# Performance work log

Measured on AMD Instinct MI355X. Metric: run time of the kernel, lower is better.

Reference implementation:

```python
import jax, jax.numpy as jnp
import numpy as np

K_H, K_W = 3, 3
STRIDE, PAD = 1, 1
GN_GROUPS = 32
EPS = 1e-5


def setup_inputs() -> dict:
    key = jax.random.key(0)
    k1, k2, k3 = jax.random.split(key, 3)
    B, C, H, W = 4, 256, 64, 64
    Cout = 256
    x = jax.random.normal(k1, (B, C, H, W), jnp.float32)
    offset = jax.random.normal(k2, (B, 2 * K_H * K_W, H, W), jnp.float32)
    weight = jax.random.normal(k3, (Cout, C, K_H, K_W), jnp.float32) * 0.02
    gamma = jnp.ones((Cout,), jnp.float32)
    beta = jnp.zeros((Cout,), jnp.float32)
    return {"x": x, "offset": offset, "weight": weight, "gamma": gamma, "beta": beta}


def _deform_conv(x, offset, weight):
    B, C, H, W = x.shape
    Cout = weight.shape[0]
    K = K_H * K_W
    Ho = (H + 2 * PAD - K_H) // STRIDE + 1
    Wo = (W + 2 * PAD - K_W) // STRIDE + 1
    ky, kx = jnp.meshgrid(jnp.arange(K_H), jnp.arange(K_W), indexing='ij')
    ky = ky.reshape(K).astype(x.dtype)
    kx = kx.reshape(K).astype(x.dtype)
    # base sampling positions per kernel tap
    py_base = (jnp.arange(Ho) * STRIDE - PAD).astype(x.dtype)[None, :] + ky[:, None]  # [K,Ho]
    px_base = (jnp.arange(Wo) * STRIDE - PAD).astype(x.dtype)[None, :] + kx[:, None]  # [K,Wo]
    off = offset.reshape(B, K, 2, Ho, Wo)  # mmcv layout: (dy, dx) pairs per tap
    py = py_base[None, :, :, None] + off[:, :, 0]  # [B,K,Ho,Wo]
    px = px_base[None, :, None, :] + off[:, :, 1]  # [B,K,Ho,Wo]
    y0 = jnp.floor(py)
    x0 = jnp.floor(px)
    ly = py - y0
    lx = px - x0
    xf = x.reshape(B, C, H * W)

    def gather(yi, xi):
        valid = (yi >= 0) & (yi <= H - 1) & (xi >= 0) & (xi <= W - 1)
        yc = jnp.clip(yi, 0, H - 1).astype(jnp.int32)
        xc = jnp.clip(xi, 0, W - 1).astype(jnp.int32)
        idx = yc * W + xc  # [B,K,Ho,Wo]
        vals = jax.vmap(lambda xb, ib: xb[:, ib])(xf, idx)  # [B,C,K,Ho,Wo]
        return vals * valid[:, None].astype(x.dtype)

    g00 = gather(y0, x0)
    g01 = gather(y0, x0 + 1)
    g10 = gather(y0 + 1, x0)
    g11 = gather(y0 + 1, x0 + 1)
    wy = ly[:, None]  # [B,1,K,Ho,Wo]
    wx = lx[:, None]
    val = ((1 - wy) * (1 - wx) * g00 + (1 - wy) * wx * g01
           + wy * (1 - wx) * g10 + wy * wx * g11)  # [B,C,K,Ho,Wo]
    return jnp.einsum('bckhw,ock->bohw', val, weight.reshape(Cout, C, K))


def reference(x, offset, weight, gamma, beta):
    y = _deform_conv(x, offset, weight)  # [B,Cout,Ho,Wo]
    B, C, H, W = y.shape
    yg = y.reshape(B, GN_GROUPS, C // GN_GROUPS, H, W)
    mean = jnp.mean(yg, axis=(2, 3, 4), keepdims=True)
    var = jnp.var(yg, axis=(2, 3, 4), keepdims=True)
    yn = ((yg - mean) * jax.lax.rsqrt(var + EPS)).reshape(B, C, H, W)
    out = yn * gamma[None, :, None, None] + beta[None, :, None, None]
    return jax.nn.relu(out)
```

## Files before the change

kernel.cpp:

```cpp
#include <hip/hip_runtime.h>

typedef unsigned short ushort_t;
typedef __bf16 bf16x8 __attribute__((ext_vector_type(8)));
typedef float f32x4 __attribute__((ext_vector_type(4)));
typedef void __attribute__((address_space(1))) gvoid_t;
typedef void __attribute__((address_space(3))) lvoid_t;

__device__ __forceinline__ float bflo(unsigned u) { return __builtin_bit_cast(float, u << 16); }
__device__ __forceinline__ float bfhi(unsigned u) { return __builtin_bit_cast(float, u & 0xffff0000u); }
__device__ __forceinline__ unsigned f2bf_bits(float f) {
  unsigned u = __builtin_bit_cast(unsigned, f);
  return (u + 0x7fffu + ((u >> 16) & 1u)) >> 16;
}
__device__ __forceinline__ ushort_t f2bf(float f) { return (ushort_t)f2bf_bits(f); }

__global__ __launch_bounds__(256) void k_prep_w(const float* __restrict__ w,
                                                ushort_t* __restrict__ wb) {
  const int idx = blockIdx.x * 256 + threadIdx.x;
  const float* src = w + (size_t)idx * 9;
  #pragma unroll
  for (int k = 0; k < 9; ++k)
    wb[(k << 16) + idx] = f2bf(src[k]);
}

__global__ __launch_bounds__(256) void k_prep_x(const float* __restrict__ x,
                                                ushort_t* __restrict__ xt) {
  __shared__ ushort_t tile[64][68];
  const int bid = blockIdx.x;
  const int b = bid >> 8;
  const int ct = (bid >> 6) & 3;
  const int pt = bid & 63;
  const int t = threadIdx.x;
  const float* xb = x + ((size_t)(b * 256 + ct * 64)) * 4096 + pt * 64;
  #pragma unroll
  for (int i = 0; i < 16; ++i) {
    const int idx = t + 256 * i;
    const int c_l = idx >> 6, p_l = idx & 63;
    tile[c_l][p_l] = f2bf(xb[(size_t)c_l * 4096 + p_l]);
  }
  __syncthreads();
  ushort_t* xo = xt + ((size_t)(b * 4096 + pt * 64)) * 256 + ct * 64;
  #pragma unroll
  for (int i = 0; i < 16; ++i) {
    const int idx = t + 256 * i;
    const int p_l = idx >> 6, c_l = idx & 63;
    xo[(size_t)p_l * 256 + c_l] = tile[c_l][p_l];
  }
}

__global__ __launch_bounds__(256) void k_gemm(const float* __restrict__ off,
                                              const ushort_t* __restrict__ xt,
                                              const ushort_t* __restrict__ wb,
                                              float* __restrict__ y) {
  __shared__ __attribute__((aligned(16))) ushort_t Abuf[64 * 64];
  __shared__ __attribute__((aligned(16))) ushort_t Bbuf[256 * 64];

  const int bid = blockIdx.x;
  const int b = bid >> 6;
  const int h = bid & 63;
  const int t = threadIdx.x;
  const int wave = t >> 6;
  const int lane = t & 63;
  const int wq = lane >> 4;
  const int wr = lane & 15;

  const int s_w = t >> 2;
  const int c4i = t & 3;

  const f32x4 zero = {0.f, 0.f, 0.f, 0.f};
  f32x4 acc[4][4];
  #pragma unroll
  for (int i = 0; i < 4; ++i)
    #pragma unroll
    for (int j = 0; j < 4; ++j) acc[i][j] = zero;

  const float* offb = off + (size_t)b * 18 * 4096 + h * 64 + s_w;
  const ushort_t* xtb = xt + (size_t)b * 4096 * 256;

  for (int k = 0; k < 9; ++k) {
    const float offy = offb[(2 * k) * 4096];
    const float offx = offb[(2 * k + 1) * 4096];
    const float py = (float)(h - 1 + k / 3) + offy;
    const float px = (float)(s_w - 1 + k % 3) + offx;
    const float fy = floorf(py), fx = floorf(px);
    const float ly = py - fy, lx = px - fx;
    const int iy0 = (int)fy, ix0 = (int)fx;
    const float vy0 = (iy0 >= 0 && iy0 < 64) ? 1.f : 0.f;
    const float vy1 = (iy0 >= -1 && iy0 < 63) ? 1.f : 0.f;
    const float vx0 = (ix0 >= 0 && ix0 < 64) ? 1.f : 0.f;
    const float vx1 = (ix0 >= -1 && ix0 < 63) ? 1.f : 0.f;
    const float w00 = (1.f - ly) * (1.f - lx) * vy0 * vx0;
    const float w01 = (1.f - ly) * lx * vy0 * vx1;
    const float w10 = ly * (1.f - lx) * vy1 * vx0;
    const float w11 = ly * lx * vy1 * vx1;
    const int cy0 = min(max(iy0, 0), 63), cy1 = min(max(iy0 + 1, 0), 63);
    const int cx0 = min(max(ix0, 0), 63), cx1 = min(max(ix0 + 1, 0), 63);
    const ushort_t* p00 = xtb + (cy0 * 64 + cx0) * 256;
    const ushort_t* p01 = xtb + (cy0 * 64 + cx1) * 256;
    const ushort_t* p10 = xtb + (cy1 * 64 + cx0) * 256;
    const ushort_t* p11 = xtb + (cy1 * 64 + cx1) * 256;

    for (int c0 = 0; c0 < 256; c0 += 64) {
      __syncthreads();
      #pragma unroll
      for (int hf = 0; hf < 2; ++hf) {
        const int cc = c0 + hf * 32 + c4i * 8;
        const uint4 q00 = *(const uint4*)(p00 + cc);
        const uint4 q01 = *(const uint4*)(p01 + cc);
        const uint4 q10 = *(const uint4*)(p10 + cc);
        const uint4 q11 = *(const uint4*)(p11 + cc);
        uint4 r;
        {
          float lo = w00 * bflo(q00.x) + w01 * bflo(q01.x) + w10 * bflo(q10.x) + w11 * bflo(q11.x);
          float hi = w00 * bfhi(q00.x) + w01 * bfhi(q01.x) + w10 * bfhi(q10.x) + w11 * bfhi(q11.x);
          r.x = f2bf_bits(lo) | (f2bf_bits(hi) << 16);
        }
        {
          float lo = w00 * bflo(q00.y) + w01 * bflo(q01.y) + w10 * bflo(q10.y) + w11 * bflo(q11.y);
          float hi = w00 * bfhi(q00.y) + w01 * bfhi(q01.y) + w10 * bfhi(q10.y) + w11 * bfhi(q11.y);
          r.y = f2bf_bits(lo) | (f2bf_bits(hi) << 16);
        }
        {
          float lo = w00 * bflo(q00.z) + w01 * bflo(q01.z) + w10 * bflo(q10.z) + w11 * bflo(q11.z);
          float hi = w00 * bfhi(q00.z) + w01 * bfhi(q01.z) + w10 * bfhi(q10.z) + w11 * bfhi(q11.z);
          r.z = f2bf_bits(lo) | (f2bf_bits(hi) << 16);
        }
        {
          float lo = w00 * bflo(q00.w) + w01 * bflo(q01.w) + w10 * bflo(q10.w) + w11 * bflo(q11.w);
          float hi = w00 * bfhi(q00.w) + w01 * bfhi(q01.w) + w10 * bfhi(q10.w) + w11 * bfhi(q11.w);
          r.w = f2bf_bits(lo) | (f2bf_bits(hi) << 16);
        }
        const int slot = (hf * 4 + c4i) ^ (s_w & 7);
        *(uint4*)&Abuf[s_w * 64 + slot * 8] = r;
      }
      #pragma unroll
      for (int i = 0; i < 8; ++i) {
        const int row = i * 32 + (t >> 3);
        const int slot = t & 7;
        const int cl = ((slot ^ (row & 7)) << 3);
        const ushort_t* g = wb + (((k << 8) + row) << 8) + c0 + cl;
        __builtin_amdgcn_global_load_lds((gvoid_t*)g,
                                         (lvoid_t*)((char*)Bbuf + i * 4096 + t * 16),
                                         16, 0, 0);
      }
      __syncthreads();
      #pragma unroll
      for (int ks = 0; ks < 2; ++ks) {
        bf16x8 af[4], bfr[4];
        #pragma unroll
        for (int tm = 0; tm < 4; ++tm) {
          const int row = tm * 16 + wr;
          const int slot = (ks * 4 + wq) ^ (row & 7);
          af[tm] = *(const bf16x8*)&Abuf[row * 64 + slot * 8];
        }
        #pragma unroll
        for (int tn = 0; tn < 4; ++tn) {
          const int row = wave * 64 + tn * 16 + wr;
          const int slot = (ks * 4 + wq) ^ (row & 7);
          bfr[tn] = *(const bf16x8*)&Bbuf[row * 64 + slot * 8];
        }
        #pragma unroll
        for (int tm = 0; tm < 4; ++tm)
          #pragma unroll
          for (int tn = 0; tn < 4; ++tn)
            acc[tm][tn] =
                __builtin_amdgcn_mfma_f32_16x16x32_bf16(af[tm], bfr[tn], acc[tm][tn], 0, 0, 0);
      }
    }
  }
  float* yb = y + ((size_t)(b * 4096 + h * 64)) * 256;
  #pragma unroll
  for (int tm = 0; tm < 4; ++tm) {
    #pragma unroll
    for (int tn = 0; tn < 4; ++tn) {
      const int o = wave * 64 + tn * 16 + wr;
      #pragma unroll
      for (int r2 = 0; r2 < 4; ++r2) {
        const int ww = tm * 16 + wq * 4 + r2;
        yb[ww * 256 + o] = acc[tm][tn][r2];
      }
    }
  }
}

__global__ __launch_bounds__(256) void k_stats(const float* __restrict__ y,
                                               float* __restrict__ stats) {
  const int bid = blockIdx.x;
  const int b = bid >> 3, ch = bid & 7;
  const int t = threadIdx.x;
  float sum = 0.f, ss = 0.f;
  const float* p = y + ((size_t)(b * 4096 + ch * 512)) * 256 + t;
  for (int s = 0; s < 512; ++s) {
    const float v = p[(size_t)s * 256];
    sum += v;
    ss += v * v;
  }
  #pragma unroll
  for (int d = 1; d < 8; d <<= 1) {
    sum += __shfl_xor(sum, d, 64);
    ss += __shfl_xor(ss, d, 64);
  }
  if ((t & 7) == 0) {
    const int g = t >> 3;
    atomicAdd(&stats[(b * 32 + g) * 2], sum);
    atomicAdd(&stats[(b * 32 + g) * 2 + 1], ss);
  }
}

__global__ __launch_bounds__(256) void k_apply(const float* __restrict__ y,
                                               const float* __restrict__ stats,
                                               const float* __restrict__ gamma,
                                               const float* __restrict__ beta,
                                               float* __restrict__ out) {
  __shared__ float tile[64][65];
  __shared__ float sm[8], sr[8], sg[64], sb[64];
  const int bid = blockIdx.x;
  const int b = bid >> 8;
  const int st = (bid >> 2) & 63;
  const int ot = bid & 3;
  const int t = threadIdx.x;
  if (t < 8) {
    const int g = ot * 8 + t;
    const float s1 = stats[(b * 32 + g) * 2];
    const float s2 = stats[(b * 32 + g) * 2 + 1];
    const float mean = s1 * (1.f / 32768.f);
    const float var = s2 * (1.f / 32768.f) - mean * mean;
    sm[t] = mean;
    sr[t] = rsqrtf(var + 1e-5f);
  }
  if (t < 64) {
    sg[t] = gamma[ot * 64 + t];
    sb[t] = beta[ot * 64 + t];
  }
  const float* yb = y + ((size_t)(b * 4096 + st * 64)) * 256 + ot * 64;
  #pragma unroll
  for (int i = 0; i < 16; ++i) {
    const int idx = t + 256 * i;
    const int s_l = idx >> 6, o_l = idx & 63;
    tile[s_l][o_l] = yb[(size_t)s_l * 256 + o_l];
  }
  __syncthreads();
  float* ob = out + ((size_t)(b * 256 + ot * 64)) * 4096 + st * 64;
  #pragma unroll
  for (int i = 0; i < 16; ++i) {
    const int idx = t + 256 * i;
    const int o_l = idx >> 6, s_l = idx & 63;
    const int g = o_l >> 3;
    float v = (tile[s_l][o_l] - sm[g]) * sr[g] * sg[o_l] + sb[o_l];
    v = v > 0.f ? v : 0.f;
    ob[(size_t)o_l * 4096 + s_l] = v;
  }
}

extern "C" void kernel_launch(void* const* d_in, const int* in_sizes, int n_in,
                              void* d_out, int out_size, void* d_ws, size_t ws_size,
                              hipStream_t stream) {
  const float* x = (const float*)d_in[0];
  const float* off = (const float*)d_in[1];
  const float* w = (const float*)d_in[2];
  const float* gamma = (const float*)d_in[3];
  const float* beta = (const float*)d_in[4];
  float* out = (float*)d_out;

  char* ws = (char*)d_ws;
  float* y = (float*)(ws);
  ushort_t* xt = (ushort_t*)(ws + 16777216);
  ushort_t* wb = (ushort_t*)(ws + 25165824);
  float* stats = (float*)(ws + 26345472);

  hipMemsetAsync(stats, 0, 1024, stream);
  k_prep_w<<<256, 256, 0, stream>>>(w, wb);
  k_prep_x<<<1024, 256, 0, stream>>>(x, xt);
  k_gemm<<<256, 256, 0, stream>>>(off, xt, wb, y);
  k_stats<<<32, 256, 0, stream>>>(y, stats);
  k_apply<<<1024, 256, 0, stream>>>(y, stats, gamma, beta, out);
}
```

Baseline: 100.6 us.

## Fuse group-norm statistics into GEMM epilogue and halve GEMM row tile

Removes the separate k_stats kernel: the GEMM epilogue now reduces per-group sum and sum of squares from its accumulators with wave shuffles and atomically adds them to the stats buffer. The GEMM tile also shrinks from 64 to 32 output pixels per block, doubling the grid to 512 blocks, which fills more of the CUs. In exchange each block reloads the full weight tile for half the output pixels, and atomic traffic on the stats buffer rises.

Result: slower. 110.1 us (+9.5%).

```diff
diff --git a/kernel.cpp b/kernel.cpp
--- a/kernel.cpp
+++ b/kernel.cpp
@@ -51,37 +51,40 @@
 __global__ __launch_bounds__(256) void k_gemm(const float* __restrict__ off,
                                               const ushort_t* __restrict__ xt,
                                               const ushort_t* __restrict__ wb,
-                                              float* __restrict__ y) {
-  __shared__ __attribute__((aligned(16))) ushort_t Abuf[64 * 64];
+                                              float* __restrict__ y,
+                                              float* __restrict__ stats) {
+  __shared__ __attribute__((aligned(16))) ushort_t Abuf[32 * 64];
   __shared__ __attribute__((aligned(16))) ushort_t Bbuf[256 * 64];
 
   const int bid = blockIdx.x;
-  const int b = bid >> 6;
-  const int h = bid & 63;
+  const int b = bid >> 7;
+  const int h = (bid >> 1) & 63;
+  const int wh = bid & 1;
   const int t = threadIdx.x;
   const int wave = t >> 6;
   const int lane = t & 63;
   const int wq = lane >> 4;
   const int wr = lane & 15;
 
-  const int s_w = t >> 2;
-  const int c4i = t & 3;
+  const int s_w = t >> 3;
+  const int c8 = t & 7;
 
   const f32x4 zero = {0.f, 0.f, 0.f, 0.f};
-  f32x4 acc[4][4];
-  #pragma unroll
-  for (int i = 0; i < 4; ++i)
+  f32x4 acc[2][4];
+  #pragma unroll
+  for (int i = 0; i < 2; ++i)
     #pragma unroll
     for (int j = 0; j < 4; ++j) acc[i][j] = zero;
 
-  const float* offb = off + (size_t)b * 18 * 4096 + h * 64 + s_w;
+  const int gw = wh * 32 + s_w;
+  const float* offb = off + (size_t)b * 18 * 4096 + h * 64 + gw;
   const ushort_t* xtb = xt + (size_t)b * 4096 * 256;
 
   for (int k = 0; k < 9; ++k) {
     const float offy = offb[(2 * k) * 4096];
     const float offx = offb[(2 * k + 1) * 4096];
     const float py = (float)(h - 1 + k / 3) + offy;
-    const float px = (float)(s_w - 1 + k % 3) + offx;
+    const float px = (float)(gw - 1 + k % 3) + offx;
     const float fy = floorf(py), fx = floorf(px);
     const float ly = py - fy, lx = px - fx;
     const int iy0 = (int)fy, ix0 = (int)fx;
@@ -102,9 +105,8 @@
 
     for (int c0 = 0; c0 < 256; c0 += 64) {
       __syncthreads();
-      #pragma unroll
-      for (int hf = 0; hf < 2; ++hf) {
-        const int cc = c0 + hf * 32 + c4i * 8;
+      {
+        const int cc = c0 + c8 * 8;
         const uint4 q00 = *(const uint4*)(p00 + cc);
         const uint4 q01 = *(const uint4*)(p01 + cc);
         const uint4 q10 = *(const uint4*)(p10 + cc);
@@ -130,7 +132,7 @@
           float hi = w00 * bfhi(q00.w) + w01 * bfhi(q01.w) + w10 * bfhi(q10.w) + w11 * bfhi(q11.w);
           r.w = f2bf_bits(lo) | (f2bf_bits(hi) << 16);
         }
-        const int slot = (hf * 4 + c4i) ^ (s_w & 7);
+        const int slot = c8 ^ (s_w & 7);
         *(uint4*)&Abuf[s_w * 64 + slot * 8] = r;
       }
       #pragma unroll
@@ -146,9 +148,9 @@
       __syncthreads();
       #pragma unroll
       for (int ks = 0; ks < 2; ++ks) {
-        bf16x8 af[4], bfr[4];
+        bf16x8 af[2], bfr[4];
         #pragma unroll
-        for (int tm = 0; tm < 4; ++tm) {
+        for (int tm = 0; tm < 2; ++tm) {
           const int row = tm * 16 + wr;
           const int slot = (ks * 4 + wq) ^ (row & 7);
           af[tm] = *(const bf16x8*)&Abuf[row * 64 + slot * 8];
@@ -160,7 +162,7 @@
           bfr[tn] = *(const bf16x8*)&Bbuf[row * 64 + slot * 8];
         }
         #pragma unroll
-        for (int tm = 0; tm < 4; ++tm)
+        for (int tm = 0; tm < 2; ++tm)
           #pragma unroll
           for (int tn = 0; tn < 4; ++tn)
             acc[tm][tn] =
@@ -168,9 +170,9 @@
       }
     }
   }
-  float* yb = y + ((size_t)(b * 4096 + h * 64)) * 256;
-  #pragma unroll
-  for (int tm = 0; tm < 4; ++tm) {
+  float* yb = y + ((size_t)(b * 4096 + h * 64 + wh * 32)) * 256;
+  #pragma unroll
+  for (int tm = 0; tm < 2; ++tm) {
     #pragma unroll
     for (int tn = 0; tn < 4; ++tn) {
       const int o = wave * 64 + tn * 16 + wr;
@@ -181,29 +183,31 @@
       }
     }
   }
-}
-
-__global__ __launch_bounds__(256) void k_stats(const float* __restrict__ y,
-                                               float* __restrict__ stats) {
-  const int bid = blockIdx.x;
-  const int b = bid >> 3, ch = bid & 7;
-  const int t = threadIdx.x;
-  float sum = 0.f, ss = 0.f;
-  const float* p = y + ((size_t)(b * 4096 + ch * 512)) * 256 + t;
-  for (int s = 0; s < 512; ++s) {
-    const float v = p[(size_t)s * 256];
-    sum += v;
-    ss += v * v;
-  }
-  #pragma unroll
-  for (int d = 1; d < 8; d <<= 1) {
-    sum += __shfl_xor(sum, d, 64);
-    ss += __shfl_xor(ss, d, 64);
-  }
-  if ((t & 7) == 0) {
-    const int g = t >> 3;
-    atomicAdd(&stats[(b * 32 + g) * 2], sum);
-    atomicAdd(&stats[(b * 32 + g) * 2 + 1], ss);
+  #pragma unroll
+  for (int tn = 0; tn < 4; ++tn) {
+    float sum = 0.f, ss = 0.f;
+    #pragma unroll
+    for (int tm = 0; tm < 2; ++tm)
+      #pragma unroll
+      for (int r2 = 0; r2 < 4; ++r2) {
+        const float v = acc[tm][tn][r2];
+        sum += v;
+        ss += v * v;
+      }
+    sum += __shfl_xor(sum, 16, 64);
+    ss += __shfl_xor(ss, 16, 64);
+    sum += __shfl_xor(sum, 32, 64);
+    ss += __shfl_xor(ss, 32, 64);
+    #pragma unroll
+    for (int d = 1; d < 8; d <<= 1) {
+      sum += __shfl_xor(sum, d, 64);
+      ss += __shfl_xor(ss, d, 64);
+    }
+    if (wq == 0 && (wr & 7) == 0) {
+      const int g = wave * 8 + tn * 2 + (wr >> 3);
+      atomicAdd(&stats[(b * 32 + g) * 2], sum);
+      atomicAdd(&stats[(b * 32 + g) * 2 + 1], ss);
+    }
   }
 }
 
@@ -271,7 +275,6 @@
   hipMemsetAsync(stats, 0, 1024, stream);
   k_prep_w<<<256, 256, 0, stream>>>(w, wb);
   k_prep_x<<<1024, 256, 0, stream>>>(x, xt);
-  k_gemm<<<256, 256, 0, stream>>>(off, xt, wb, y);
-  k_stats<<<32, 256, 0, stream>>>(y, stats);
+  k_gemm<<<512, 256, 0, stream>>>(off, xt, wb, y, stats);
   k_apply<<<1024, 256, 0, stream>>>(y, stats, gamma, beta, out);
 }
```
